# Kernel optimization log

Measured on AMD Instinct MI355X. Metric: run time of the kernel, lower is better.

The kernel has to match this reference:

```python
import jax, jax.numpy as jnp
import numpy as np

M, NQ, NK, DX, H, HD, DT, KH = 2, 1024, 1024, 512, 8, 64, 2, 32
SCALE = HD ** -0.5


def setup_inputs() -> dict:
    key = jax.random.key(0)
    ks = jax.random.split(key, 12)
    w = lambda k, shape: jax.random.normal(k, shape, jnp.float32) * 0.02
    return dict(
        xq=jax.random.normal(ks[0], (M, NQ, DX), jnp.float32),
        xk=jax.random.normal(ks[1], (M, NK, DX), jnp.float32),
        xv=jax.random.normal(ks[2], (M, NK, DX), jnp.float32),
        tq=jax.random.normal(ks[3], (M, NQ, DT), jnp.float32),
        tk=jax.random.normal(ks[4], (M, NK, DT), jnp.float32),
        Wq=w(ks[5], (DX, H * HD)),
        Wk=w(ks[6], (DX, H * HD)),
        Wv=w(ks[7], (DX, H * HD)),
        Wo=w(ks[8], (H * HD, DX)),
        bo=jnp.zeros((DX,), jnp.float32),
        K1=w(ks[9], (DT, KH)),
        kb1=jnp.zeros((KH,), jnp.float32),
        K2=w(ks[10], (KH, H)),
        kb2=jnp.zeros((H,), jnp.float32),
    )


def _heads(t):
    # [b, n, h*d] -> [b, h, n, d]
    b, n, _ = t.shape
    return t.reshape(b, n, H, HD).transpose(0, 2, 1, 3)


def reference(xq, xk, xv, tq, tk, Wq, Wk, Wv, Wo, bo, K1, kb1, K2, kb2):
    q = _heads(xq @ Wq)            # [m,h,nq,d]
    k = _heads(xk @ Wk)            # [m,h,nk,d]
    token_dots = jnp.einsum('bhqd,bhkd->bhqk', q, k) * SCALE
    # diagonal attention term: query attends to its own (key/value-projected) token
    xq_k = _heads(xq @ Wk)
    diag_dots = jnp.sum(q * xq_k, axis=-1, keepdims=True) * SCALE   # [m,h,nq,1]
    token_dots = jnp.concatenate([token_dots, diag_dots], axis=-1)  # [m,h,nq,nk+1]
    # translation group action: pairwise differences, plus zero diagonal diff
    diff = tq[:, :, None, :] - tk[:, None, :, :]                    # [m,nq,nk,dt]
    diff = jnp.concatenate([diff, jnp.zeros((M, NQ, 1, DT), diff.dtype)], axis=2)
    # kernel network (MLP) -> per-head relative-position bias [m,nq,nk+1,h]
    kd = jax.nn.relu(diff @ K1 + kb1) @ K2 + kb2
    dots = token_dots + kd.transpose(0, 3, 1, 2)                    # [m,h,nq,nk+1]
    attn = jax.nn.softmax(dots, axis=-1)
    v = _heads(xv @ Wv)
    xq_v = _heads(xq @ Wv)
    out = jnp.einsum('bhqk,bhkd->bhqd', attn[..., :-1], v) + attn[..., -1:] * xq_v
    out = out.transpose(0, 2, 1, 3).reshape(M, NQ, H * HD) @ Wo + bo
    # phi_t is None -> tq_new = tq
    return (out, tq)
```

## Files before the change

kernel.cpp:

```cpp
#include <hip/hip_runtime.h>
#include <hip/hip_bf16.h>
#include <cstddef>

typedef __attribute__((ext_vector_type(8))) short bf16x8;
typedef __attribute__((ext_vector_type(4))) float f32x4;

constexpr int NH  = 8;
constexpr int HHD = 512;
constexpr int KHC = 32;
constexpr float SCALE_F = 0.125f;
constexpr int KSPLIT = 4;

__device__ __forceinline__ unsigned short f2bf(float f) {
    unsigned int u = __builtin_bit_cast(unsigned int, f);
    u = (u + 0x7FFFu + ((u >> 16) & 1u)) >> 16;
    return (unsigned short)u;
}
__device__ __forceinline__ float bf2f(unsigned short h) {
    unsigned int u = ((unsigned int)h) << 16;
    return __builtin_bit_cast(float, u);
}
__device__ __forceinline__ unsigned int cvt_pk_bf16(float lo, float hi) {
    unsigned int r;
    asm("v_cvt_pk_bf16_f32 %0, %1, %2" : "=v"(r) : "v"(lo), "v"(hi));
    return r;
}

struct PrepAll {
    const float* xs[3]; unsigned short* xd[3];
    const float* wsrc[4]; unsigned short* wdst[4];
    const float* tq; const float* tk;
    const float* K1; const float* kb1;
    float* Aa; float* Bb;
};
__global__ __launch_bounds__(256) void prep_all(PrepAll c) {
    __shared__ unsigned short Ts[64][66];
    const int b = blockIdx.x;
    const int t = threadIdx.x;

    if (b < 1536) {
        const int z = b / 512;
        const size_t i8 = ((size_t)(b - z * 512) * 256 + t) * 8;
        const float4 f0 = *(const float4*)(c.xs[z] + i8);
        const float4 f1 = *(const float4*)(c.xs[z] + i8 + 4);
        ushort4 o0, o1;
        o0.x = f2bf(f0.x); o0.y = f2bf(f0.y); o0.z = f2bf(f0.z); o0.w = f2bf(f0.w);
        o1.x = f2bf(f1.x); o1.y = f2bf(f1.y); o1.z = f2bf(f1.z); o1.w = f2bf(f1.w);
        *(ushort4*)(c.xd[z] + i8) = o0;
        *(ushort4*)(c.xd[z] + i8 + 4) = o1;
    } else if (b < 1792) {
        const int bb = b - 1536;
        const int z = bb >> 6;
        const int rem = bb & 63;
        const int k0 = (rem & 7) * 64, j0 = (rem >> 3) * 64;
        const float* W = c.wsrc[z];
        unsigned short* Wt = c.wdst[z];
        {
            const int kr = t >> 2;
            const int jc = (t & 3) * 16;
            const float* g = W + (size_t)(k0 + kr) * 512 + j0 + jc;
            #pragma unroll
            for (int i4 = 0; i4 < 4; ++i4) {
                float4 f = *(const float4*)(g + i4 * 4);
                Ts[kr][jc + i4 * 4 + 0] = f2bf(f.x);
                Ts[kr][jc + i4 * 4 + 1] = f2bf(f.y);
                Ts[kr][jc + i4 * 4 + 2] = f2bf(f.z);
                Ts[kr][jc + i4 * 4 + 3] = f2bf(f.w);
            }
        }
        __syncthreads();
        {
            const int j = t >> 2;
            const int kseg = (t & 3) * 16;
            unsigned short tmp[16];
            #pragma unroll
            for (int i = 0; i < 16; ++i) tmp[i] = Ts[kseg + i][j];
            unsigned short* g = Wt + (size_t)(j0 + j) * 512 + k0 + kseg;
            #pragma unroll
            for (int i4 = 0; i4 < 4; ++i4)
                *(ushort4*)(g + i4 * 4) = *(ushort4*)&tmp[i4 * 4];
        }
    } else {
        const int idx = (b - 1792) * 256 + t;
        const int which = idx >> 16;
        const int e = idx & 65535;
        const int row = e >> 5;
        const int j = e & 31;
        const float* tt = which ? c.tk : c.tq;
        float v = tt[row * 2 + 0] * c.K1[j] + tt[row * 2 + 1] * c.K1[KHC + j];
        if (!which) v += c.kb1[j];
        (which ? c.Bb : c.Aa)[e] = v;
    }
}

__device__ __forceinline__ void mfma_gemm_core(const unsigned short* __restrict__ A,
                                               const unsigned short* __restrict__ Bt,
                                               int r0, int c0, f32x4 acc[2][4])
{
    __shared__ __align__(16) char As[16384];
    __shared__ __align__(16) char Bs[8192];

    const int tid = threadIdx.x;
    const int l = tid & 63, w = tid >> 6;
    const int lw = l & 15, lg = l >> 4;

    #pragma unroll
    for (int r = 0; r < 2; ++r)
        #pragma unroll
        for (int cb = 0; cb < 4; ++cb) acc[r][cb] = (f32x4){0.f, 0.f, 0.f, 0.f};

    const int arow_s = tid >> 1;
    const int ahalf  = tid & 1;
    const int brow_s = tid >> 2;
    const int bseg   = tid & 3;

    for (int kb = 0; kb < 512; kb += 64) {
        __syncthreads();
        {
            const unsigned short* g = A + (size_t)(r0 + arow_s) * 512 + kb + ahalf * 32;
            const int base = arow_s * 128 + ahalf * 64;
            const int sw = (arow_s & 7) << 4;
            #pragma unroll
            for (int i = 0; i < 4; ++i)
                *(float4*)(As + ((base + i * 16) ^ sw)) = *(const float4*)(g + i * 8);
        }
        {
            const unsigned short* g = Bt + (size_t)(c0 + brow_s) * 512 + kb + bseg * 16;
            const int base = brow_s * 128 + bseg * 32;
            const int sw = (brow_s & 7) << 4;
            #pragma unroll
            for (int i = 0; i < 2; ++i)
                *(float4*)(Bs + ((base + i * 16) ^ sw)) = *(const float4*)(g + i * 8);
        }
        __syncthreads();

        bf16x8 bfrag[4][2];
        #pragma unroll
        for (int cb = 0; cb < 4; ++cb) {
            const int bcol = cb * 16 + lw;
            const int sw = (bcol & 7) << 4;
            bfrag[cb][0] = *(const bf16x8*)(Bs + ((bcol * 128 + lg * 16) ^ sw));
            bfrag[cb][1] = *(const bf16x8*)(Bs + ((bcol * 128 + 64 + lg * 16) ^ sw));
        }
        #pragma unroll
        for (int r = 0; r < 2; ++r) {
            const int arow = w * 32 + r * 16 + lw;
            const int sw = (arow & 7) << 4;
            bf16x8 a0 = *(const bf16x8*)(As + ((arow * 128 + lg * 16) ^ sw));
            bf16x8 a1 = *(const bf16x8*)(As + ((arow * 128 + 64 + lg * 16) ^ sw));
            #pragma unroll
            for (int cb = 0; cb < 4; ++cb) {
                acc[r][cb] = __builtin_amdgcn_mfma_f32_16x16x32_bf16(a0, bfrag[cb][0], acc[r][cb], 0, 0, 0);
                acc[r][cb] = __builtin_amdgcn_mfma_f32_16x16x32_bf16(a1, bfrag[cb][1], acc[r][cb], 0, 0, 0);
            }
        }
    }
}

struct Proj5 {
    const unsigned short* A[5];
    const unsigned short* B[5];
    unsigned short* O[5];
    unsigned short* VT;
};

__global__ __launch_bounds__(256) void proj_mfma(Proj5 p) {
    const int z = blockIdx.z;
    const int r0 = blockIdx.x * 128, c0 = blockIdx.y * 64;
    f32x4 acc[2][4];
    mfma_gemm_core(p.A[z], p.B[z], r0, c0, acc);

    const int l = threadIdx.x & 63, w = threadIdx.x >> 6;
    const int lw = l & 15, lg = l >> 4;
    #pragma unroll
    for (int r = 0; r < 2; ++r)
        #pragma unroll
        for (int cb = 0; cb < 4; ++cb) {
            const int gc = c0 + cb * 16 + lw;
            const int h = gc >> 6, d = gc & 63;
            #pragma unroll
            for (int rr = 0; rr < 4; ++rr) {
                const int gr = r0 + w * 32 + r * 16 + lg * 4 + rr;
                const int m = gr >> 10, n = gr & 1023;
                const unsigned short v = f2bf(acc[r][cb][rr]);
                if (z == 2)
                    p.VT[(((size_t)m * NH + h) * 64 + d) * 1024 + n] = v;
                else
                    p.O[z][(((size_t)m * NH + h) * 1024 + n) * 64 + d] = v;
            }
        }
}

__global__ __launch_bounds__(256) void outproj_mfma(const unsigned short* __restrict__ A,
                                                    const unsigned short* __restrict__ Bt,
                                                    const float* __restrict__ bias,
                                                    float* __restrict__ C) {
    const int r0 = blockIdx.x * 128, c0 = blockIdx.y * 64;
    f32x4 acc[2][4];
    mfma_gemm_core(A, Bt, r0, c0, acc);

    const int l = threadIdx.x & 63, w = threadIdx.x >> 6;
    const int lw = l & 15, lg = l >> 4;
    #pragma unroll
    for (int r = 0; r < 2; ++r)
        #pragma unroll
        for (int cb = 0; cb < 4; ++cb) {
            const int gc = c0 + cb * 16 + lw;
            const float bv = bias[gc];
            #pragma unroll
            for (int rr = 0; rr < 4; ++rr) {
                const int gr = r0 + w * 32 + r * 16 + lg * 4 + rr;
                C[(size_t)gr * HHD + gc] = acc[r][cb][rr] + bv;
            }
        }
}

__global__ __launch_bounds__(256) void bias_mfma(const float* __restrict__ Aa,
                                                 const float* __restrict__ Bb,
                                                 const float* __restrict__ K2,
                                                 const float* __restrict__ kb2,
                                                 unsigned short* __restrict__ kd)
{
    const int tid = threadIdx.x;
    const int l = tid & 63;
    const int kb = tid >> 6;
    const int lw = l & 15, lg = l >> 4;
    const int bid = blockIdx.x;
    const int kt = bid & 15;
    const int qg = (bid >> 4) & 63;
    const int m  = bid >> 10;

    float k2f[8];
    #pragma unroll
    for (int e = 0; e < 8; ++e)
        k2f[e] = (lw < 8) ? K2[(lg * 8 + e) * 8 + lw] : 0.f;
    union { unsigned int u[4]; bf16x8 v; } bu;
    #pragma unroll
    for (int i = 0; i < 4; ++i) bu.u[i] = cvt_pk_bf16(k2f[2 * i], k2f[2 * i + 1]);
    const bf16x8 bfrag = bu.v;

    const float c0 = (lw < 8) ? kb2[lw] : 0.f;
    const f32x4 cini = {c0, c0, c0, c0};

    const int kglob = kt * 64 + kb * 16 + lw;
    const float* bp = Bb + ((size_t)m * 1024 + kglob) * 32 + lg * 8;
    const float4 b0 = *(const float4*)bp;
    const float4 b1 = *(const float4*)(bp + 4);
    const float bl[8] = {b0.x, b0.y, b0.z, b0.w, b1.x, b1.y, b1.z, b1.w};

    const float* arow = Aa + ((size_t)m * 1024 + qg * 16) * 32 + lg * 8;
    unsigned short* kout = kd + (size_t)(m * 8 + lw) * 1048576
                         + qg * 16384 + kt * 1024 + kb * 256 + lg * 64;

    #pragma unroll
    for (int t = 0; t < 16; t += 2) {
        const float4 a00 = *(const float4*)(arow + (size_t)t * 32);
        const float4 a01 = *(const float4*)(arow + (size_t)t * 32 + 4);
        union { unsigned int u[4]; bf16x8 v; } r0u;
        r0u.u[0] = cvt_pk_bf16(fmaxf(a00.x - bl[0], 0.f), fmaxf(a00.y - bl[1], 0.f));
        r0u.u[1] = cvt_pk_bf16(fmaxf(a00.z - bl[2], 0.f), fmaxf(a00.w - bl[3], 0.f));
        r0u.u[2] = cvt_pk_bf16(fmaxf(a01.x - bl[4], 0.f), fmaxf(a01.y - bl[5], 0.f));
        r0u.u[3] = cvt_pk_bf16(fmaxf(a01.z - bl[6], 0.f), fmaxf(a01.w - bl[7], 0.f));
        const f32x4 d0 = __builtin_amdgcn_mfma_f32_16x16x32_bf16(r0u.v, bfrag, cini, 0, 0, 0);

        const float4 a10 = *(const float4*)(arow + (size_t)(t + 1) * 32);
        const float4 a11 = *(const float4*)(arow + (size_t)(t + 1) * 32 + 4);
        union { unsigned int u[4]; bf16x8 v; } r1u;
        r1u.u[0] = cvt_pk_bf16(fmaxf(a10.x - bl[0], 0.f), fmaxf(a10.y - bl[1], 0.f));
        r1u.u[1] = cvt_pk_bf16(fmaxf(a10.z - bl[2], 0.f), fmaxf(a10.w - bl[3], 0.f));
        r1u.u[2] = cvt_pk_bf16(fmaxf(a11.x - bl[4], 0.f), fmaxf(a11.y - bl[5], 0.f));
        r1u.u[3] = cvt_pk_bf16(fmaxf(a11.z - bl[6], 0.f), fmaxf(a11.w - bl[7], 0.f));
        const f32x4 d1 = __builtin_amdgcn_mfma_f32_16x16x32_bf16(r1u.v, bfrag, cini, 0, 0, 0);

        if (lw < 8) {
            uint4 o;
            o.x = cvt_pk_bf16(d0[0], d0[1]);
            o.y = cvt_pk_bf16(d0[2], d0[3]);
            o.z = cvt_pk_bf16(d1[0], d1[1]);
            o.w = cvt_pk_bf16(d1[2], d1[3]);
            *(uint4*)(kout + t * 4) = o;
        }
    }
}

__global__ __launch_bounds__(256, 4) void attn_mfma(
    const unsigned short* __restrict__ qh, const unsigned short* __restrict__ kh,
    const unsigned short* __restrict__ vt, const unsigned short* __restrict__ kd,
    float* __restrict__ pacc, float* __restrict__ pl)
{
    __shared__ __align__(16) char Ksh[8192];
    __shared__ __align__(16) char Vsh[8192];
    __shared__ __align__(16) char Psh[4][2048];

    const int tid = threadIdx.x;
    const int l = tid & 63;
    const int w = tid >> 6;
    const int lw = l & 15, lg = l >> 4;
    const int qt = blockIdx.x;
    const int mh = blockIdx.y;
    const int ks = blockIdx.z;
    const int q0 = qt * 64;

    const int qrow = q0 + w * 16 + lw;
    const unsigned short* qp = qh + ((size_t)mh * 1024 + qrow) * 64;
    const bf16x8 qf0 = *(const bf16x8*)(qp + lg * 8);
    const bf16x8 qf1 = *(const bf16x8*)(qp + 32 + lg * 8);

    f32x4 oacc[4] = {{0.f,0.f,0.f,0.f},{0.f,0.f,0.f,0.f},
                     {0.f,0.f,0.f,0.f},{0.f,0.f,0.f,0.f}};
    float lsum = 0.f;

    const int srow = tid >> 2;
    const int scol = (tid & 3) * 32;
    const int ssw  = (srow & 7) << 4;

    char* pbase = Psh[w];
    const int prsw = (lw & 7) << 4;
    const size_t kdwave = (((size_t)mh * 64 + qt * 4 + w) * 16 + ks * 4) * 1024;

    for (int kt = 0; kt < 4; ++kt) {
        const int k0 = ks * 256 + kt * 64;
        __syncthreads();
        {
            const char* g = (const char*)(kh + ((size_t)mh * 1024 + k0 + srow) * 64) + scol;
            const int a = srow * 128 + scol;
            *(float4*)(Ksh + (a ^ ssw))        = *(const float4*)g;
            *(float4*)(Ksh + ((a + 16) ^ ssw)) = *(const float4*)(g + 16);
        }
        {
            const char* g = (const char*)(vt + ((size_t)mh * 64 + srow) * 1024 + k0) + scol;
            const int a = srow * 128 + scol;
            *(float4*)(Vsh + (a ^ ssw))        = *(const float4*)g;
            *(float4*)(Vsh + ((a + 16) ^ ssw)) = *(const float4*)(g + 16);
        }
        __syncthreads();

        const unsigned short* kdt = kd + kdwave + (size_t)kt * 1024;
        #pragma unroll
        for (int kb = 0; kb < 4; ++kb) {
            f32x4 s = {0.f, 0.f, 0.f, 0.f};
            const int row = kb * 16 + lw;
            const int rsw = (row & 7) << 4;
            const int a0 = row * 128 + lg * 16;
            bf16x8 af0 = *(const bf16x8*)(Ksh + (a0 ^ rsw));
            s = __builtin_amdgcn_mfma_f32_16x16x32_bf16(af0, qf0, s, 0, 0, 0);
            bf16x8 af1 = *(const bf16x8*)(Ksh + ((a0 + 64) ^ rsw));
            s = __builtin_amdgcn_mfma_f32_16x16x32_bf16(af1, qf1, s, 0, 0, 0);

            ushort4 bb = *(const ushort4*)(kdt + kb * 256 + l * 4);
            float p0 = __expf(fmaf(s[0], SCALE_F, bf2f(bb.x)));
            float p1 = __expf(fmaf(s[1], SCALE_F, bf2f(bb.y)));
            float p2 = __expf(fmaf(s[2], SCALE_F, bf2f(bb.z)));
            float p3 = __expf(fmaf(s[3], SCALE_F, bf2f(bb.w)));
            lsum += (p0 + p1) + (p2 + p3);

            unsigned int u0 = f2bf(p0) | ((unsigned int)f2bf(p1) << 16);
            unsigned int u1 = f2bf(p2) | ((unsigned int)f2bf(p3) << 16);
            const int pa = lw * 128 + kb * 32 + lg * 8;
            *(uint2*)(pbase + (pa ^ prsw)) = make_uint2(u0, u1);
        }

        #pragma unroll
        for (int kc = 0; kc < 2; ++kc) {
            const int pa = lw * 128 + kc * 64 + lg * 16;
            bf16x8 pfrag = *(const bf16x8*)(pbase + (pa ^ prsw));
            #pragma unroll
            for (int db = 0; db < 4; ++db) {
                const int vrow = db * 16 + lw;
                const int va = vrow * 128 + kc * 64 + lg * 16;
                bf16x8 vfrag = *(const bf16x8*)(Vsh + (va ^ ((vrow & 7) << 4)));
                oacc[db] = __builtin_amdgcn_mfma_f32_16x16x32_bf16(pfrag, vfrag, oacc[db], 0, 0, 0);
            }
        }
    }

    lsum += __shfl_xor(lsum, 16, 64);
    lsum += __shfl_xor(lsum, 32, 64);

    float* pr = pacc + (((size_t)mh * KSPLIT + ks) * 1024) * 64;
    #pragma unroll
    for (int r = 0; r < 4; ++r) {
        const int qo = q0 + w * 16 + lg * 4 + r;
        float* rowp = pr + (size_t)qo * 64 + lw;
        rowp[0]  = oacc[0][r];
        rowp[16] = oacc[1][r];
        rowp[32] = oacc[2][r];
        rowp[48] = oacc[3][r];
    }
    if (lg == 0)
        pl[((size_t)mh * KSPLIT + ks) * 1024 + q0 + w * 16 + lw] = lsum;
}

__global__ __launch_bounds__(256) void reduce_k(
    const float* __restrict__ pacc, const float* __restrict__ pl,
    const unsigned short* __restrict__ qg, const unsigned short* __restrict__ xqk,
    const unsigned short* __restrict__ xqv, const float* __restrict__ K2,
    const float* __restrict__ kb1, const float* __restrict__ kb2,
    unsigned short* __restrict__ attn_out)
{
    const int rowid = blockIdx.x * 4 + (threadIdx.x >> 6);
    const int d = threadIdx.x & 63;
    const int mh = rowid >> 10;
    const int q = rowid & 1023;
    const int m = mh >> 3;
    const int h = mh & 7;

    float accsum = 0.f, lsumv = 0.f;
    #pragma unroll
    for (int kc = 0; kc < KSPLIT; ++kc) {
        accsum += pacc[(((size_t)mh * KSPLIT + kc) * 1024 + q) * 64 + d];
        lsumv  += pl[((size_t)mh * KSPLIT + kc) * 1024 + q];
    }
    const size_t ro = ((size_t)mh * 1024 + q) * 64 + d;
    float s = bf2f(qg[ro]) * bf2f(xqk[ro]);
    #pragma unroll
    for (int off = 32; off > 0; off >>= 1) s += __shfl_xor(s, off, 64);
    float bias_d = kb2[h];
    #pragma unroll
    for (int j = 0; j < KHC; ++j) bias_d += fmaxf(kb1[j], 0.f) * K2[j * NH + h];
    const float pd = __expf(fmaf(s, SCALE_F, bias_d));
    const float outv = (accsum + pd * bf2f(xqv[ro])) / (lsumv + pd);
    attn_out[((size_t)(m * 1024 + q)) * HHD + h * 64 + d] = f2bf(outv);
}

extern "C" void kernel_launch(void* const* d_in, const int* in_sizes, int n_in,
                              void* d_out, int out_size, void* d_ws, size_t ws_size,
                              hipStream_t stream)
{
    const float* xq  = (const float*)d_in[0];
    const float* xk  = (const float*)d_in[1];
    const float* xv  = (const float*)d_in[2];
    const float* tq  = (const float*)d_in[3];
    const float* tk  = (const float*)d_in[4];
    const float* Wq  = (const float*)d_in[5];
    const float* Wk  = (const float*)d_in[6];
    const float* Wv  = (const float*)d_in[7];
    const float* Wo  = (const float*)d_in[8];
    const float* bo  = (const float*)d_in[9];
    const float* K1  = (const float*)d_in[10];
    const float* kb1 = (const float*)d_in[11];
    const float* K2  = (const float*)d_in[12];
    const float* kb2 = (const float*)d_in[13];

    char* ws = (char*)d_ws;
    unsigned short* qh   = (unsigned short*)(ws);
    unsigned short* kh   = (unsigned short*)(ws +  2097152);
    unsigned short* vtp  = (unsigned short*)(ws +  4194304);
    unsigned short* xqk  = (unsigned short*)(ws +  6291456);
    unsigned short* xqv  = (unsigned short*)(ws +  8388608);
    float*          Aa   = (float*)(ws + 10485760);
    float*          Bb   = (float*)(ws + 10747904);
    unsigned short* kd   = (unsigned short*)(ws + 11010048);
    float*          pacc = (float*)(ws + 44564480);
    float*          pl   = (float*)(ws + 61341696);
    unsigned short* Wot  = (unsigned short*)(ws + 61603840);
    unsigned short* xa   = (unsigned short*)(ws + 11010048);
    unsigned short* xb   = (unsigned short*)(ws + 13107200);
    unsigned short* xc   = (unsigned short*)(ws + 15204352);
    unsigned short* Wqt  = (unsigned short*)(ws + 17301504);
    unsigned short* Wkt  = (unsigned short*)(ws + 17825792);
    unsigned short* Wvt  = (unsigned short*)(ws + 18350080);
    unsigned short* aout = (unsigned short*)(ws + 11010048);
    float*          outp = (float*)d_out;

    PrepAll pa;
    pa.xs[0] = xq; pa.xs[1] = xk; pa.xs[2] = xv;
    pa.xd[0] = xa; pa.xd[1] = xb; pa.xd[2] = xc;
    pa.wsrc[0] = Wq; pa.wsrc[1] = Wk; pa.wsrc[2] = Wv; pa.wsrc[3] = Wo;
    pa.wdst[0] = Wqt; pa.wdst[1] = Wkt; pa.wdst[2] = Wvt; pa.wdst[3] = Wot;
    pa.tq = tq; pa.tk = tk; pa.K1 = K1; pa.kb1 = kb1; pa.Aa = Aa; pa.Bb = Bb;
    hipLaunchKernelGGL(prep_all, dim3(2304), dim3(256), 0, stream, pa);

    Proj5 p;
    p.A[0] = xa; p.B[0] = Wqt; p.O[0] = qh;
    p.A[1] = xb; p.B[1] = Wkt; p.O[1] = kh;
    p.A[2] = xc; p.B[2] = Wvt; p.O[2] = nullptr;
    p.A[3] = xa; p.B[3] = Wkt; p.O[3] = xqk;
    p.A[4] = xa; p.B[4] = Wvt; p.O[4] = xqv;
    p.VT = vtp;
    hipLaunchKernelGGL(proj_mfma, dim3(16, 8, 5), dim3(256), 0, stream, p);

    hipLaunchKernelGGL(bias_mfma, dim3(2048), dim3(256), 0, stream, Aa, Bb, K2, kb2, kd);

    hipLaunchKernelGGL(attn_mfma, dim3(16, 16, KSPLIT), dim3(256), 0, stream,
                       qh, kh, vtp, kd, pacc, pl);

    hipLaunchKernelGGL(reduce_k, dim3(4096), dim3(256), 0, stream,
                       pacc, pl, qh, xqk, xqv, K2, kb1, kb2, aout);

    hipLaunchKernelGGL(outproj_mfma, dim3(16, 8, 1), dim3(256), 0, stream, aout, Wot, bo, outp);

    hipMemcpyAsync(outp + 1048576, tq, 4096 * sizeof(float),
                   hipMemcpyDeviceToDevice, stream);
}
```

Before: 160.6 us.

## Fuse projection GEMMs with bias MLP kernel and enlarge GEMM tiles to 128x128

Merges the five projection GEMMs and the relative-position bias MLP into one launch, with the first 320 blocks doing projections and the rest computing the bias. The GEMM core moves from 128x64 to 128x128 tiles with a 2x2 wave layout, which raises per-block reuse and halves the outproj grid. The projection inputs are relocated to new workspace offsets, because the bias output (kd) overlaps the old ones and the two stages now run concurrently. The cost is fewer GEMM blocks, more registers per block, and mixed block types within one launch.

```diff
diff --git a/kernel.cpp b/kernel.cpp
--- a/kernel.cpp
+++ b/kernel.cpp
@@ -93,43 +93,42 @@
     }
 }
 
-__device__ __forceinline__ void mfma_gemm_core(const unsigned short* __restrict__ A,
-                                               const unsigned short* __restrict__ Bt,
-                                               int r0, int c0, f32x4 acc[2][4])
+__device__ __forceinline__ void mfma_core_128(const unsigned short* __restrict__ A,
+                                              const unsigned short* __restrict__ Bt,
+                                              int r0, int c0, f32x4 acc[4][4])
 {
     __shared__ __align__(16) char As[16384];
-    __shared__ __align__(16) char Bs[8192];
+    __shared__ __align__(16) char Bs[16384];
 
     const int tid = threadIdx.x;
     const int l = tid & 63, w = tid >> 6;
     const int lw = l & 15, lg = l >> 4;
+    const int wr = (w >> 1) * 64, wc = (w & 1) * 64;
 
     #pragma unroll
-    for (int r = 0; r < 2; ++r)
+    for (int r = 0; r < 4; ++r)
         #pragma unroll
         for (int cb = 0; cb < 4; ++cb) acc[r][cb] = (f32x4){0.f, 0.f, 0.f, 0.f};
 
-    const int arow_s = tid >> 1;
-    const int ahalf  = tid & 1;
-    const int brow_s = tid >> 2;
-    const int bseg   = tid & 3;
+    const int row_s = tid >> 1;
+    const int half  = tid & 1;
 
     for (int kb = 0; kb < 512; kb += 64) {
         __syncthreads();
         {
-            const unsigned short* g = A + (size_t)(r0 + arow_s) * 512 + kb + ahalf * 32;
-            const int base = arow_s * 128 + ahalf * 64;
-            const int sw = (arow_s & 7) << 4;
+            const unsigned short* g = A + (size_t)(r0 + row_s) * 512 + kb + half * 32;
+            const int base = row_s * 128 + half * 64;
+            const int sw = (row_s & 7) << 4;
             #pragma unroll
             for (int i = 0; i < 4; ++i)
                 *(float4*)(As + ((base + i * 16) ^ sw)) = *(const float4*)(g + i * 8);
         }
         {
-            const unsigned short* g = Bt + (size_t)(c0 + brow_s) * 512 + kb + bseg * 16;
-            const int base = brow_s * 128 + bseg * 32;
-            const int sw = (brow_s & 7) << 4;
-            #pragma unroll
-            for (int i = 0; i < 2; ++i)
+            const unsigned short* g = Bt + (size_t)(c0 + row_s) * 512 + kb + half * 32;
+            const int base = row_s * 128 + half * 64;
+            const int sw = (row_s & 7) << 4;
+            #pragma unroll
+            for (int i = 0; i < 4; ++i)
                 *(float4*)(Bs + ((base + i * 16) ^ sw)) = *(const float4*)(g + i * 8);
         }
         __syncthreads();
@@ -137,14 +136,14 @@
         bf16x8 bfrag[4][2];
         #pragma unroll
         for (int cb = 0; cb < 4; ++cb) {
-            const int bcol = cb * 16 + lw;
+            const int bcol = wc + cb * 16 + lw;
             const int sw = (bcol & 7) << 4;
             bfrag[cb][0] = *(const bf16x8*)(Bs + ((bcol * 128 + lg * 16) ^ sw));
             bfrag[cb][1] = *(const bf16x8*)(Bs + ((bcol * 128 + 64 + lg * 16) ^ sw));
         }
         #pragma unroll
-        for (int r = 0; r < 2; ++r) {
-            const int arow = w * 32 + r * 16 + lw;
+        for (int r = 0; r < 4; ++r) {
+            const int arow = wr + r * 16 + lw;
             const int sw = (arow & 7) << 4;
             bf16x8 a0 = *(const bf16x8*)(As + ((arow * 128 + lg * 16) ^ sw));
             bf16x8 a1 = *(const bf16x8*)(As + ((arow * 128 + 64 + lg * 16) ^ sw));
@@ -157,130 +156,132 @@
     }
 }
 
-struct Proj5 {
+struct ProjBias {
     const unsigned short* A[5];
     const unsigned short* B[5];
     unsigned short* O[5];
     unsigned short* VT;
+    const float* Aa; const float* Bb;
+    const float* K2; const float* kb2;
+    unsigned short* kd;
 };
 
-__global__ __launch_bounds__(256) void proj_mfma(Proj5 p) {
-    const int z = blockIdx.z;
-    const int r0 = blockIdx.x * 128, c0 = blockIdx.y * 64;
-    f32x4 acc[2][4];
-    mfma_gemm_core(p.A[z], p.B[z], r0, c0, acc);
-
-    const int l = threadIdx.x & 63, w = threadIdx.x >> 6;
+__global__ __launch_bounds__(256) void projbias(ProjBias p) {
+    const int b = blockIdx.x;
+    const int tid = threadIdx.x;
+    const int l = tid & 63;
     const int lw = l & 15, lg = l >> 4;
-    #pragma unroll
-    for (int r = 0; r < 2; ++r)
-        #pragma unroll
-        for (int cb = 0; cb < 4; ++cb) {
-            const int gc = c0 + cb * 16 + lw;
-            const int h = gc >> 6, d = gc & 63;
-            #pragma unroll
-            for (int rr = 0; rr < 4; ++rr) {
-                const int gr = r0 + w * 32 + r * 16 + lg * 4 + rr;
-                const int m = gr >> 10, n = gr & 1023;
-                const unsigned short v = f2bf(acc[r][cb][rr]);
-                if (z == 2)
-                    p.VT[(((size_t)m * NH + h) * 64 + d) * 1024 + n] = v;
-                else
-                    p.O[z][(((size_t)m * NH + h) * 1024 + n) * 64 + d] = v;
+
+    if (b < 320) {
+        const int z = b >> 6;
+        const int t = b & 63;
+        const int r0 = (t >> 2) * 128, c0 = (t & 3) * 128;
+        f32x4 acc[4][4];
+        mfma_core_128(p.A[z], p.B[z], r0, c0, acc);
+
+        const int w = tid >> 6;
+        const int wr = (w >> 1) * 64, wc = (w & 1) * 64;
+        #pragma unroll
+        for (int r = 0; r < 4; ++r)
+            #pragma unroll
+            for (int cb = 0; cb < 4; ++cb) {
+                const int gc = c0 + wc + cb * 16 + lw;
+                const int h = gc >> 6, d = gc & 63;
+                #pragma unroll
+                for (int rr = 0; rr < 4; ++rr) {
+                    const int gr = r0 + wr + r * 16 + lg * 4 + rr;
+                    const int m = gr >> 10, n = gr & 1023;
+                    const unsigned short v = f2bf(acc[r][cb][rr]);
+                    if (z == 2)
+                        p.VT[(((size_t)m * NH + h) * 64 + d) * 1024 + n] = v;
+                    else
+                        p.O[z][(((size_t)m * NH + h) * 1024 + n) * 64 + d] = v;
+                }
             }
-        }
+    } else {
+        const int bb = b - 320;
+        const int kb = tid >> 6;
+        const int kt = bb & 15;
+        const int qg = (bb >> 4) & 63;
+        const int m  = bb >> 10;
+
+        float k2f[8];
+        #pragma unroll
+        for (int e = 0; e < 8; ++e)
+            k2f[e] = (lw < 8) ? p.K2[(lg * 8 + e) * 8 + lw] : 0.f;
+        union { unsigned int u[4]; bf16x8 v; } bu;
+        #pragma unroll
+        for (int i = 0; i < 4; ++i) bu.u[i] = cvt_pk_bf16(k2f[2 * i], k2f[2 * i + 1]);
+        const bf16x8 bfrag = bu.v;
+
+        const float c0v = (lw < 8) ? p.kb2[lw] : 0.f;
+        const f32x4 cini = {c0v, c0v, c0v, c0v};
+
+        const int kglob = kt * 64 + kb * 16 + lw;
+        const float* bp = p.Bb + ((size_t)m * 1024 + kglob) * 32 + lg * 8;
+        const float4 b0 = *(const float4*)bp;
+        const float4 b1 = *(const float4*)(bp + 4);
+        const float bl[8] = {b0.x, b0.y, b0.z, b0.w, b1.x, b1.y, b1.z, b1.w};
+
+        const float* arow = p.Aa + ((size_t)m * 1024 + qg * 16) * 32 + lg * 8;
+        unsigned short* kout = p.kd + (size_t)(m * 8 + lw) * 1048576
+                             + qg * 16384 + kt * 1024 + kb * 256 + lg * 64;
+
+        #pragma unroll
+        for (int t = 0; t < 16; t += 2) {
+            const float4 a00 = *(const float4*)(arow + (size_t)t * 32);
+            const float4 a01 = *(const float4*)(arow + (size_t)t * 32 + 4);
+            union { unsigned int u[4]; bf16x8 v; } r0u;
+            r0u.u[0] = cvt_pk_bf16(fmaxf(a00.x - bl[0], 0.f), fmaxf(a00.y - bl[1], 0.f));
+            r0u.u[1] = cvt_pk_bf16(fmaxf(a00.z - bl[2], 0.f), fmaxf(a00.w - bl[3], 0.f));
+            r0u.u[2] = cvt_pk_bf16(fmaxf(a01.x - bl[4], 0.f), fmaxf(a01.y - bl[5], 0.f));
+            r0u.u[3] = cvt_pk_bf16(fmaxf(a01.z - bl[6], 0.f), fmaxf(a01.w - bl[7], 0.f));
+            const f32x4 d0 = __builtin_amdgcn_mfma_f32_16x16x32_bf16(r0u.v, bfrag, cini, 0, 0, 0);
+
+            const float4 a10 = *(const float4*)(arow + (size_t)(t + 1) * 32);
+            const float4 a11 = *(const float4*)(arow + (size_t)(t + 1) * 32 + 4);
+            union { unsigned int u[4]; bf16x8 v; } r1u;
+            r1u.u[0] = cvt_pk_bf16(fmaxf(a10.x - bl[0], 0.f), fmaxf(a10.y - bl[1], 0.f));
+            r1u.u[1] = cvt_pk_bf16(fmaxf(a10.z - bl[2], 0.f), fmaxf(a10.w - bl[3], 0.f));
+            r1u.u[2] = cvt_pk_bf16(fmaxf(a11.x - bl[4], 0.f), fmaxf(a11.y - bl[5], 0.f));
+            r1u.u[3] = cvt_pk_bf16(fmaxf(a11.z - bl[6], 0.f), fmaxf(a11.w - bl[7], 0.f));
+            const f32x4 d1 = __builtin_amdgcn_mfma_f32_16x16x32_bf16(r1u.v, bfrag, cini, 0, 0, 0);
+
+            if (lw < 8) {
+                uint4 o;
+                o.x = cvt_pk_bf16(d0[0], d0[1]);
+                o.y = cvt_pk_bf16(d0[2], d0[3]);
+                o.z = cvt_pk_bf16(d1[0], d1[1]);
+                o.w = cvt_pk_bf16(d1[2], d1[3]);
+                *(uint4*)(kout + t * 4) = o;
+            }
+        }
+    }
 }
 
 __global__ __launch_bounds__(256) void outproj_mfma(const unsigned short* __restrict__ A,
                                                     const unsigned short* __restrict__ Bt,
                                                     const float* __restrict__ bias,
                                                     float* __restrict__ C) {
-    const int r0 = blockIdx.x * 128, c0 = blockIdx.y * 64;
-    f32x4 acc[2][4];
-    mfma_gemm_core(A, Bt, r0, c0, acc);
+    const int r0 = blockIdx.x * 128, c0 = blockIdx.y * 128;
+    f32x4 acc[4][4];
+    mfma_core_128(A, Bt, r0, c0, acc);
 
     const int l = threadIdx.x & 63, w = threadIdx.x >> 6;
     const int lw = l & 15, lg = l >> 4;
+    const int wr = (w >> 1) * 64, wc = (w & 1) * 64;
     #pragma unroll
-    for (int r = 0; r < 2; ++r)
+    for (int r = 0; r < 4; ++r)
         #pragma unroll
         for (int cb = 0; cb < 4; ++cb) {
-            const int gc = c0 + cb * 16 + lw;
+            const int gc = c0 + wc + cb * 16 + lw;
             const float bv = bias[gc];
             #pragma unroll
             for (int rr = 0; rr < 4; ++rr) {
-                const int gr = r0 + w * 32 + r * 16 + lg * 4 + rr;
+                const int gr = r0 + wr + r * 16 + lg * 4 + rr;
                 C[(size_t)gr * HHD + gc] = acc[r][cb][rr] + bv;
             }
         }
-}
-
-__global__ __launch_bounds__(256) void bias_mfma(const float* __restrict__ Aa,
-                                                 const float* __restrict__ Bb,
-                                                 const float* __restrict__ K2,
-                                                 const float* __restrict__ kb2,
-                                                 unsigned short* __restrict__ kd)
-{
-    const int tid = threadIdx.x;
-    const int l = tid & 63;
-    const int kb = tid >> 6;
-    const int lw = l & 15, lg = l >> 4;
-    const int bid = blockIdx.x;
-    const int kt = bid & 15;
-    const int qg = (bid >> 4) & 63;
-    const int m  = bid >> 10;
-
-    float k2f[8];
-    #pragma unroll
-    for (int e = 0; e < 8; ++e)
-        k2f[e] = (lw < 8) ? K2[(lg * 8 + e) * 8 + lw] : 0.f;
-    union { unsigned int u[4]; bf16x8 v; } bu;
-    #pragma unroll
-    for (int i = 0; i < 4; ++i) bu.u[i] = cvt_pk_bf16(k2f[2 * i], k2f[2 * i + 1]);
-    const bf16x8 bfrag = bu.v;
-
-    const float c0 = (lw < 8) ? kb2[lw] : 0.f;
-    const f32x4 cini = {c0, c0, c0, c0};
-
-    const int kglob = kt * 64 + kb * 16 + lw;
-    const float* bp = Bb + ((size_t)m * 1024 + kglob) * 32 + lg * 8;
-    const float4 b0 = *(const float4*)bp;
-    const float4 b1 = *(const float4*)(bp + 4);
-    const float bl[8] = {b0.x, b0.y, b0.z, b0.w, b1.x, b1.y, b1.z, b1.w};
-
-    const float* arow = Aa + ((size_t)m * 1024 + qg * 16) * 32 + lg * 8;
-    unsigned short* kout = kd + (size_t)(m * 8 + lw) * 1048576
-                         + qg * 16384 + kt * 1024 + kb * 256 + lg * 64;
-
-    #pragma unroll
-    for (int t = 0; t < 16; t += 2) {
-        const float4 a00 = *(const float4*)(arow + (size_t)t * 32);
-        const float4 a01 = *(const float4*)(arow + (size_t)t * 32 + 4);
-        union { unsigned int u[4]; bf16x8 v; } r0u;
-        r0u.u[0] = cvt_pk_bf16(fmaxf(a00.x - bl[0], 0.f), fmaxf(a00.y - bl[1], 0.f));
-        r0u.u[1] = cvt_pk_bf16(fmaxf(a00.z - bl[2], 0.f), fmaxf(a00.w - bl[3], 0.f));
-        r0u.u[2] = cvt_pk_bf16(fmaxf(a01.x - bl[4], 0.f), fmaxf(a01.y - bl[5], 0.f));
-        r0u.u[3] = cvt_pk_bf16(fmaxf(a01.z - bl[6], 0.f), fmaxf(a01.w - bl[7], 0.f));
-        const f32x4 d0 = __builtin_amdgcn_mfma_f32_16x16x32_bf16(r0u.v, bfrag, cini, 0, 0, 0);
-
-        const float4 a10 = *(const float4*)(arow + (size_t)(t + 1) * 32);
-        const float4 a11 = *(const float4*)(arow + (size_t)(t + 1) * 32 + 4);
-        union { unsigned int u[4]; bf16x8 v; } r1u;
-        r1u.u[0] = cvt_pk_bf16(fmaxf(a10.x - bl[0], 0.f), fmaxf(a10.y - bl[1], 0.f));
-        r1u.u[1] = cvt_pk_bf16(fmaxf(a10.z - bl[2], 0.f), fmaxf(a10.w - bl[3], 0.f));
-        r1u.u[2] = cvt_pk_bf16(fmaxf(a11.x - bl[4], 0.f), fmaxf(a11.y - bl[5], 0.f));
-        r1u.u[3] = cvt_pk_bf16(fmaxf(a11.z - bl[6], 0.f), fmaxf(a11.w - bl[7], 0.f));
-        const f32x4 d1 = __builtin_amdgcn_mfma_f32_16x16x32_bf16(r1u.v, bfrag, cini, 0, 0, 0);
-
-        if (lw < 8) {
-            uint4 o;
-            o.x = cvt_pk_bf16(d0[0], d0[1]);
-            o.y = cvt_pk_bf16(d0[2], d0[3]);
-            o.z = cvt_pk_bf16(d1[0], d1[1]);
-            o.w = cvt_pk_bf16(d1[2], d1[3]);
-            *(uint4*)(kout + t * 4) = o;
-        }
-    }
 }
 
 __global__ __launch_bounds__(256, 4) void attn_mfma(
@@ -463,24 +464,31 @@
     unsigned short* aout = (unsigned short*)(ws + 11010048);
     float*          outp = (float*)d_out;
 
+    unsigned short* xa2  = (unsigned short*)(ws + 62128128);
+    unsigned short* xb2  = (unsigned short*)(ws + 64225280);
+    unsigned short* xc2  = (unsigned short*)(ws + 66322432);
+    unsigned short* Wqt2 = (unsigned short*)(ws + 68419584);
+    unsigned short* Wkt2 = (unsigned short*)(ws + 68943872);
+    unsigned short* Wvt2 = (unsigned short*)(ws + 69468160);
+    (void)xa; (void)xb; (void)xc; (void)Wqt; (void)Wkt; (void)Wvt;
+
     PrepAll pa;
     pa.xs[0] = xq; pa.xs[1] = xk; pa.xs[2] = xv;
-    pa.xd[0] = xa; pa.xd[1] = xb; pa.xd[2] = xc;
+    pa.xd[0] = xa2; pa.xd[1] = xb2; pa.xd[2] = xc2;
     pa.wsrc[0] = Wq; pa.wsrc[1] = Wk; pa.wsrc[2] = Wv; pa.wsrc[3] = Wo;
-    pa.wdst[0] = Wqt; pa.wdst[1] = Wkt; pa.wdst[2] = Wvt; pa.wdst[3] = Wot;
+    pa.wdst[0] = Wqt2; pa.wdst[1] = Wkt2; pa.wdst[2] = Wvt2; pa.wdst[3] = Wot;
     pa.tq = tq; pa.tk = tk; pa.K1 = K1; pa.kb1 = kb1; pa.Aa = Aa; pa.Bb = Bb;
     hipLaunchKernelGGL(prep_all, dim3(2304), dim3(256), 0, stream, pa);
 
-    Proj5 p;
-    p.A[0] = xa; p.B[0] = Wqt; p.O[0] = qh;
-    p.A[1] = xb; p.B[1] = Wkt; p.O[1] = kh;
-    p.A[2] = xc; p.B[2] = Wvt; p.O[2] = nullptr;
-    p.A[3] = xa; p.B[3] = Wkt; p.O[3] = xqk;
-    p.A[4] = xa; p.B[4] = Wvt; p.O[4] = xqv;
-    p.VT = vtp;
-    hipLaunchKernelGGL(proj_mfma, dim3(16, 8, 5), dim3(256), 0, stream, p);
-
-    hipLaunchKernelGGL(bias_mfma, dim3(2048), dim3(256), 0, stream, Aa, Bb, K2, kb2, kd);
+    ProjBias pb;
+    pb.A[0] = xa2; pb.B[0] = Wqt2; pb.O[0] = qh;
+    pb.A[1] = xb2; pb.B[1] = Wkt2; pb.O[1] = kh;
+    pb.A[2] = xc2; pb.B[2] = Wvt2; pb.O[2] = nullptr;
+    pb.A[3] = xa2; pb.B[3] = Wkt2; pb.O[3] = xqk;
+    pb.A[4] = xa2; pb.B[4] = Wvt2; pb.O[4] = xqv;
+    pb.VT = vtp;
+    pb.Aa = Aa; pb.Bb = Bb; pb.K2 = K2; pb.kb2 = kb2; pb.kd = kd;
+    hipLaunchKernelGGL(projbias, dim3(2368), dim3(256), 0, stream, pb);
 
     hipLaunchKernelGGL(attn_mfma, dim3(16, 16, KSPLIT), dim3(256), 0, stream,
                        qh, kh, vtp, kd, pacc, pl);
@@ -488,7 +496,7 @@
     hipLaunchKernelGGL(reduce_k, dim3(4096), dim3(256), 0, stream,
                        pacc, pl, qh, xqk, xqv, K2, kb1, kb2, aout);
 
-    hipLaunchKernelGGL(outproj_mfma, dim3(16, 8, 1), dim3(256), 0, stream, aout, Wot, bo, outp);
+    hipLaunchKernelGGL(outproj_mfma, dim3(16, 4, 1), dim3(256), 0, stream, aout, Wot, bo, outp);
 
     hipMemcpyAsync(outp + 1048576, tq, 4096 * sizeof(float),
                    hipMemcpyDeviceToDevice, stream);
```

Measured after the change: 159.1 us. No clear change (-0.9%).
